# Optimization experiments

Measured on AMD Instinct MI355X. Metric: run time of the kernel, lower is better.

The kernel has to match this reference:

```python
import jax, jax.numpy as jnp
import numpy as np

N, M, P = 100000, 20000, 1600000          # nodes, hyperedges, incidence pairs
C_IN, HID, OUT = 768, 128, 16             # OUT = n_layers = n_classes
EPS = 1e-5


def setup_inputs() -> dict:
    key = jax.random.key(0)
    ks = jax.random.split(key, 8)
    X = jax.random.normal(ks[0], (N, C_IN), jnp.float32)
    v_idx = jax.random.randint(ks[1], (P,), 0, N)
    e_idx = jax.random.randint(ks[2], (P,), 0, M)
    # parameters
    W_enc = jax.random.normal(ks[3], (C_IN, HID), jnp.float32) / np.sqrt(C_IN).astype(np.float32)
    b_enc = jnp.zeros((HID,), jnp.float32)
    ln_g = jnp.ones((OUT, HID), jnp.float32)
    ln_b = jnp.zeros((OUT, HID), jnp.float32)
    Wt = jax.random.normal(ks[4], (OUT, HID, HID), jnp.float32) / np.sqrt(HID).astype(np.float32)
    bt = jnp.zeros((OUT, HID), jnp.float32)
    W_out = jax.random.normal(ks[5], (HID, OUT), jnp.float32) / np.sqrt(HID).astype(np.float32)
    b_out = jnp.zeros((OUT,), jnp.float32)
    return dict(X=X, v_idx=v_idx, e_idx=e_idx, W_enc=W_enc, b_enc=b_enc,
                ln_g=ln_g, ln_b=ln_b, Wt=Wt, bt=bt, W_out=W_out, b_out=b_out)


def reference(X, v_idx, e_idx, W_enc, b_enc, ln_g, ln_b, Wt, bt, W_out, b_out):
    seg = jax.ops.segment_sum
    ones = jnp.ones((P,), X.dtype)
    inv_ce = 1.0 / jnp.maximum(seg(ones, e_idx, num_segments=M), 1.0)  # 1/|e|
    inv_cv = 1.0 / jnp.maximum(seg(ones, v_idx, num_segments=N), 1.0)  # 1/deg(v)

    def layernorm(h, g, b):
        mu = jnp.mean(h, axis=-1, keepdims=True)
        var = jnp.var(h, axis=-1, keepdims=True)
        return (h - mu) * jax.lax.rsqrt(var + EPS) * g + b

    def v2v_mean(h):
        # vertex -> hyperedge mean, then hyperedge -> vertex mean (HGNN+)
        Xe = seg(h[v_idx], e_idx, num_segments=M) * inv_ce[:, None]   # [M, HID]
        return seg(Xe[e_idx], v_idx, num_segments=N) * inv_cv[:, None]  # [N, HID]

    x = X @ W_enc + b_enc  # node_encoder

    def step(x, params):
        g, b, W, bb = params
        h = jax.nn.relu(layernorm(x, g, b))  # res+ block: norm -> act -> dropout(eval noop)
        h = h @ W + bb                       # HGNNPConv theta
        h = v2v_mean(h)                      # hypergraph message passing
        h = jax.nn.relu(h)                   # conv act (conv dropout = eval noop)
        return x + h, None                   # residual

    x, _ = jax.lax.scan(step, x, (ln_g, ln_b, Wt, bt))
    return jax.nn.log_softmax(x @ W_out + b_out, axis=1)
```

## Files before the change

kernel.cpp:

```cpp
#include <hip/hip_runtime.h>
#include <cstdint>
#include <cstddef>

#define N_NODES 100000
#define M_EDGES 20000
#define P_PAIRS 1600000
#define CIN 768
#define HID 128
#define OUT_C 16
#define NLAYERS 16
#define LN_EPS 1e-5f

using half8  = __attribute__((ext_vector_type(8))) _Float16;
using half4v = __attribute__((ext_vector_type(4))) _Float16;
using half2v = __attribute__((ext_vector_type(2))) _Float16;
using f32x4  = __attribute__((ext_vector_type(4))) float;
using f32x2  = __attribute__((ext_vector_type(2))) float;

#if defined(__has_builtin)
#if __has_builtin(__builtin_amdgcn_cvt_pk_f32_fp8) && __has_builtin(__builtin_amdgcn_cvt_pk_fp8_f32)
#define HAVE_HW_FP8 1
#endif
#endif

#ifndef HAVE_HW_FP8
#include <hip/hip_fp8.h>
#endif


__device__ __forceinline__ void acc4w(float* acc, unsigned w) {
#ifdef HAVE_HW_FP8
    f32x2 lo = __builtin_amdgcn_cvt_pk_f32_fp8((int)w, false);
    f32x2 hi = __builtin_amdgcn_cvt_pk_f32_fp8((int)w, true);
    acc[0] += lo[0]; acc[1] += lo[1]; acc[2] += hi[0]; acc[3] += hi[1];
#else
#pragma unroll
    for (int i = 0; i < 4; i++) {
        __half_raw hr = __hip_cvt_fp8_to_halfraw((__hip_fp8_storage_t)((w >> (8 * i)) & 0xffu), __HIP_E4M3);
        acc[i] += __half2float(*(__half*)&hr);
    }
#endif
}

__device__ __forceinline__ void acc16v(float* acc, uint4 w) {
    acc4w(acc + 0,  w.x);
    acc4w(acc + 4,  w.y);
    acc4w(acc + 8,  w.z);
    acc4w(acc + 12, w.w);
}

__device__ __forceinline__ unsigned char f32_to_fp8(float v) {
#ifdef HAVE_HW_FP8
    return (unsigned char)(__builtin_amdgcn_cvt_pk_fp8_f32(v, v, 0, false) & 0xff);
#else
    return (unsigned char)__hip_cvt_float_to_fp8(v, __HIP_SATFINITE, __HIP_E4M3);
#endif
}

__device__ __forceinline__ unsigned short pack2_fp8(float a, float b) {
#ifdef HAVE_HW_FP8
    return (unsigned short)(__builtin_amdgcn_cvt_pk_fp8_f32(a, b, 0, false) & 0xffff);
#else
    return (unsigned short)((unsigned)f32_to_fp8(a) | ((unsigned)f32_to_fp8(b) << 8));
#endif
}

__device__ __forceinline__ unsigned pack4_fp8(float a, float b, float c, float d) {
#ifdef HAVE_HW_FP8
    int w = __builtin_amdgcn_cvt_pk_fp8_f32(a, b, 0, false);
    w = __builtin_amdgcn_cvt_pk_fp8_f32(c, d, w, true);
    return (unsigned)w;
#else
    return (unsigned)f32_to_fp8(a) | ((unsigned)f32_to_fp8(b) << 8) |
           ((unsigned)f32_to_fp8(c) << 16) | ((unsigned)f32_to_fp8(d) << 24);
#endif
}


__global__ void hist_kernel(const int* __restrict__ v_idx, const int* __restrict__ e_idx,
                            unsigned* __restrict__ cnt_v, unsigned* __restrict__ cnt_e) {
    int p = blockIdx.x * 256 + threadIdx.x;
    if (p < P_PAIRS) {
        atomicAdd(&cnt_v[v_idx[p]], 1u);
        atomicAdd(&cnt_e[e_idx[p]], 1u);
    }
}

#define SCAN_EPT 16
#define SCAN_CHUNK 4096

__global__ void scan_block_sums(const unsigned* __restrict__ cnt, int n,
                                unsigned* __restrict__ bsum) {
    __shared__ unsigned ws[4];
    int t = threadIdx.x;
    int base = blockIdx.x * SCAN_CHUNK + t * SCAN_EPT;
    unsigned s = 0;
#pragma unroll
    for (int i = 0; i < SCAN_EPT; i++) {
        int idx = base + i;
        if (idx < n) s += cnt[idx];
    }
#pragma unroll
    for (int off = 1; off < 64; off <<= 1) s += __shfl_xor(s, off);
    int lane = t & 63, w = t >> 6;
    if (lane == 0) ws[w] = s;
    __syncthreads();
    if (t == 0) bsum[blockIdx.x] = ws[0] + ws[1] + ws[2] + ws[3];
}

__global__ void scan_tops(const unsigned* __restrict__ bsum, int B,
                          unsigned* __restrict__ bbase, unsigned* __restrict__ total_out) {
    int t = threadIdx.x;
    unsigned v = (t < B) ? bsum[t] : 0u;
    unsigned s = v;
#pragma unroll
    for (int off = 1; off < 64; off <<= 1) {
        unsigned u = __shfl_up(s, off);
        if (t >= off) s += u;
    }
    if (t < B) bbase[t] = s - v;
    if (t == 63) *total_out = s;
}

__global__ void scan_final(const unsigned* __restrict__ cnt, int n,
                           const unsigned* __restrict__ bbase,
                           unsigned* __restrict__ offs, unsigned* __restrict__ cur,
                           float* __restrict__ inv) {
    __shared__ unsigned wtot[4];
    int t = threadIdx.x;
    int lane = t & 63, w = t >> 6;
    int base = blockIdx.x * SCAN_CHUNK + t * SCAN_EPT;
    unsigned vals[SCAN_EPT];
    unsigned tsum = 0;
#pragma unroll
    for (int i = 0; i < SCAN_EPT; i++) {
        int idx = base + i;
        unsigned v = (idx < n) ? cnt[idx] : 0u;
        vals[i] = v;
        tsum += v;
    }
    unsigned s = tsum;
#pragma unroll
    for (int off = 1; off < 64; off <<= 1) {
        unsigned u = __shfl_up(s, off);
        if (lane >= off) s += u;
    }
    unsigned texcl = s - tsum;
    if (lane == 63) wtot[w] = s;
    __syncthreads();
    unsigned wbase = 0;
    for (int i = 0; i < w; i++) wbase += wtot[i];
    unsigned run = bbase[blockIdx.x] + wbase + texcl;
#pragma unroll
    for (int i = 0; i < SCAN_EPT; i++) {
        int idx = base + i;
        if (idx < n) {
            offs[idx] = run;
            cur[idx] = run;
            unsigned c = vals[i];
            inv[idx] = 1.0f / (float)(c > 1u ? c : 1u);
            run += c;
        }
    }
}


__global__ void fill_v_kernel(const int* __restrict__ v_idx, const int* __restrict__ e_idx,
                              unsigned* __restrict__ cur_v, unsigned short* __restrict__ vert_nbr) {
    int p = blockIdx.x * 256 + threadIdx.x;
    if (p < P_PAIRS) {
        unsigned s = atomicAdd(&cur_v[v_idx[p]], 1u);
        vert_nbr[s] = (unsigned short)e_idx[p];
    }
}

__global__ void fill_e_kernel(const int* __restrict__ v_idx, const int* __restrict__ e_idx,
                              unsigned* __restrict__ cur_e, int* __restrict__ edge_nbr) {
    int p = blockIdx.x * 256 + threadIdx.x;
    if (p < P_PAIRS) {
        unsigned s = atomicAdd(&cur_e[e_idx[p]], 1u);
        edge_nbr[s] = v_idx[p];
    }
}


__global__ void convert_wT_kernel(const float* __restrict__ W, _Float16* __restrict__ WT,
                                  int K) {
    const float* src = W + (size_t)blockIdx.y * K * 128;
    _Float16* dst = WT + (size_t)blockIdx.y * K * 128;
    int idx = blockIdx.x * 256 + threadIdx.x;
    if (idx < K * 128) {
        int k = idx >> 7, n = idx & 127;
        dst[(size_t)n * K + k] = (_Float16)src[idx];
    }
}


#define BK  64
#define LDK 72

template<bool A_FP32, int OMODE>
__global__ __launch_bounds__(256) void mfma_gemm_kernel(
    const void* __restrict__ Ap, const _Float16* __restrict__ Bt,
    const float* __restrict__ bias, void* __restrict__ outp,
    int nrows, int K) {
    __shared__ _Float16 Asm[128 * LDK];
    __shared__ _Float16 Bsm[128 * LDK];
    int tid = threadIdx.x;
    int row0 = blockIdx.x * 128;
    int lane = tid & 63, wave = tid >> 6;
    int wy = wave >> 1, wx = wave & 1;
    int m16 = lane & 15, quad = lane >> 4;

    f32x4 acc[4][4];
#pragma unroll
    for (int r = 0; r < 4; r++)
#pragma unroll
        for (int c = 0; c < 4; c++) acc[r][c] = (f32x4)0.f;

    float bv[4];
#pragma unroll
    for (int c = 0; c < 4; c++) bv[c] = bias[wx * 64 + c * 16 + m16];

    for (int k0 = 0; k0 < K; k0 += BK) {
        __syncthreads();
        if (A_FP32) {
            const float* A = (const float*)Ap;
#pragma unroll
            for (int i = 0; i < 8; i++) {
                int idx = tid + i * 256;
                int r = idx >> 4, c = idx & 15;
                int rg = row0 + r; if (rg >= nrows) rg = nrows - 1;
                float4 v = *(const float4*)(A + (size_t)rg * K + k0 + c * 4);
                half4v h = { (_Float16)v.x, (_Float16)v.y, (_Float16)v.z, (_Float16)v.w };
                *(half4v*)&Asm[r * LDK + c * 4] = h;
            }
        } else {
            const _Float16* A = (const _Float16*)Ap;
#pragma unroll
            for (int i = 0; i < 4; i++) {
                int idx = tid + i * 256;
                int r = idx >> 3, c = idx & 7;
                int rg = row0 + r; if (rg >= nrows) rg = nrows - 1;
                half8 v = *(const half8*)(A + (size_t)rg * K + k0 + c * 8);
                *(half8*)&Asm[r * LDK + c * 8] = v;
            }
        }
#pragma unroll
        for (int i = 0; i < 4; i++) {
            int idx = tid + i * 256;
            int r = idx >> 3, c = idx & 7;
            half8 v = *(const half8*)(Bt + (size_t)r * K + k0 + c * 8);
            *(half8*)&Bsm[r * LDK + c * 8] = v;
        }
        __syncthreads();
#pragma unroll
        for (int ks = 0; ks < 2; ks++) {
            half8 af[4], bf[4];
#pragma unroll
            for (int r = 0; r < 4; r++)
                af[r] = *(half8*)&Asm[(wy * 64 + r * 16 + m16) * LDK + ks * 32 + quad * 8];
#pragma unroll
            for (int c = 0; c < 4; c++)
                bf[c] = *(half8*)&Bsm[(wx * 64 + c * 16 + m16) * LDK + ks * 32 + quad * 8];
#pragma unroll
            for (int r = 0; r < 4; r++)
#pragma unroll
                for (int c = 0; c < 4; c++)
                    acc[r][c] = __builtin_amdgcn_mfma_f32_16x16x32_f16(af[r], bf[c], acc[r][c], 0, 0, 0);
        }
    }
#pragma unroll
    for (int r = 0; r < 4; r++) {
#pragma unroll
        for (int v = 0; v < 4; v++) {
            int m = wy * 64 + r * 16 + quad * 4 + v;
            int row = row0 + m;
            if (row < nrows) {
#pragma unroll
                for (int c = 0; c < 4; c++) {
                    int n = wx * 64 + c * 16 + m16;
                    float val = acc[r][c][v] + bv[c];
                    if (OMODE == 0) {
                        ((float*)outp)[(size_t)row * HID + n] = val;
                    } else {
                        ((unsigned char*)outp)[(size_t)row * HID + n] = f32_to_fp8(val);
                    }
                }
            }
        }
    }
}


__global__ __launch_bounds__(256) void ln_relu_kernel(const float* __restrict__ x,
                                                      const float* __restrict__ g,
                                                      const float* __restrict__ b,
                                                      unsigned char* __restrict__ a8) {
    int row = (blockIdx.x * 256 + threadIdx.x) >> 6;
    int lane = threadIdx.x & 63;
    if (row >= N_NODES) return;
    float2 v = *(const float2*)(x + (size_t)row * HID + 2 * lane);
    float s = v.x + v.y;
#pragma unroll
    for (int off = 1; off < 64; off <<= 1) s += __shfl_xor(s, off);
    float mu = s * (1.0f / 128.0f);
    float d0 = v.x - mu, d1 = v.y - mu;
    float q = d0 * d0 + d1 * d1;
#pragma unroll
    for (int off = 1; off < 64; off <<= 1) q += __shfl_xor(q, off);
    float rstd = rsqrtf(q * (1.0f / 128.0f) + LN_EPS);
    float2 gg = *(const float2*)(g + 2 * lane);
    float2 bb = *(const float2*)(b + 2 * lane);
    float h0 = fmaxf(d0 * rstd * gg.x + bb.x, 0.f);
    float h1 = fmaxf(d1 * rstd * gg.y + bb.y, 0.f);
    *(unsigned short*)(a8 + (size_t)row * HID + 2 * lane) = pack2_fp8(h0, h1);
}


__global__ __launch_bounds__(256) void edge_agg_kernel(const unsigned char* __restrict__ a8,
                                                       const int* __restrict__ edge_nbr,
                                                       const unsigned* __restrict__ offs,
                                                       const float* __restrict__ inv_ce,
                                                       _Float16* __restrict__ Ae) {
    int m = blockIdx.x * 4 + (threadIdx.x >> 6);
    int lane = threadIdx.x & 63;
    int g = lane >> 3, t = lane & 7;
    unsigned beg = offs[m], end = offs[m + 1];
    float acc[16];
#pragma unroll
    for (int i = 0; i < 16; i++) acc[i] = 0.f;
    const unsigned char* base = a8 + t * 16;
    unsigned j = beg;
    for (; j + 16 <= end; j += 16) {
        int v0 = edge_nbr[j + g];
        int v1 = edge_nbr[j + 8 + g];
        uint4 w0 = *(const uint4*)(base + (size_t)v0 * HID);
        uint4 w1 = *(const uint4*)(base + (size_t)v1 * HID);
        acc16v(acc, w0);
        acc16v(acc, w1);
    }
    if (j + 8 <= end) {
        int v0 = edge_nbr[j + g];
        uint4 w0 = *(const uint4*)(base + (size_t)v0 * HID);
        acc16v(acc, w0);
        j += 8;
    }
    if (j < end) {
        unsigned idx = j + g;
        bool val = idx < end;
        int v0 = edge_nbr[val ? idx : beg];
        uint4 w = *(const uint4*)(base + (size_t)v0 * HID);
        if (!val) { w.x = 0; w.y = 0; w.z = 0; w.w = 0; }
        acc16v(acc, w);
    }
#pragma unroll
    for (int i = 0; i < 16; i++) {
        acc[i] += __shfl_xor(acc[i], 8);
        acc[i] += __shfl_xor(acc[i], 16);
        acc[i] += __shfl_xor(acc[i], 32);
    }
    if (lane < 8) {
        float ic = inv_ce[m];
        half8 o0, o1;
#pragma unroll
        for (int i = 0; i < 8; i++) o0[i] = (_Float16)(acc[i] * ic);
#pragma unroll
        for (int i = 0; i < 8; i++) o1[i] = (_Float16)(acc[8 + i] * ic);
        *(half8*)(Ae + (size_t)m * HID + t * 16) = o0;
        *(half8*)(Ae + (size_t)m * HID + t * 16 + 8) = o1;
    }
}


__global__ __launch_bounds__(256) void vert_fused_kernel(
    const unsigned char* __restrict__ Xe8, const unsigned short* __restrict__ vert_nbr,
    const unsigned* __restrict__ offs, const float* __restrict__ inv_cv,
    float* __restrict__ x, const float* __restrict__ gw, const float* __restrict__ bw,
    unsigned char* __restrict__ a8, int do_ln) {
    int v = blockIdx.x * 4 + (threadIdx.x >> 6);
    int lane = threadIdx.x & 63;
    int g = lane >> 3, t = lane & 7;
    unsigned beg = offs[v], end = offs[v + 1];
    float acc[16];
#pragma unroll
    for (int i = 0; i < 16; i++) acc[i] = 0.f;
    const unsigned char* base = Xe8 + t * 16;
    unsigned j = beg;
    for (; j + 16 <= end; j += 16) {
        int e0 = vert_nbr[j + g];
        int e1 = vert_nbr[j + 8 + g];
        uint4 w0 = *(const uint4*)(base + (size_t)e0 * HID);
        uint4 w1 = *(const uint4*)(base + (size_t)e1 * HID);
        acc16v(acc, w0);
        acc16v(acc, w1);
    }
    if (j + 8 <= end) {
        int e0 = vert_nbr[j + g];
        uint4 w0 = *(const uint4*)(base + (size_t)e0 * HID);
        acc16v(acc, w0);
        j += 8;
    }
    if (j < end) {
        unsigned idx = j + g;
        bool val = idx < end;
        int e0 = vert_nbr[val ? idx : beg];
        uint4 w = *(const uint4*)(base + (size_t)e0 * HID);
        if (!val) { w.x = 0; w.y = 0; w.z = 0; w.w = 0; }
        acc16v(acc, w);
    }
#pragma unroll
    for (int i = 0; i < 16; i++) {
        acc[i] += __shfl_xor(acc[i], 8);
        acc[i] += __shfl_xor(acc[i], 16);
        acc[i] += __shfl_xor(acc[i], 32);
    }
    if (lane < 8) {
        float ic = inv_cv[v];
        float xv[16];
        f32x4* xp = (f32x4*)(x + (size_t)v * HID + t * 16);
        f32x4 xa = xp[0], xb = xp[1], xc = xp[2], xd = xp[3];
#pragma unroll
        for (int i = 0; i < 4; i++) { xv[i] = xa[i]; xv[4 + i] = xb[i]; xv[8 + i] = xc[i]; xv[12 + i] = xd[i]; }
#pragma unroll
        for (int i = 0; i < 16; i++) xv[i] += fmaxf(acc[i] * ic, 0.f);
#pragma unroll
        for (int i = 0; i < 4; i++) { xa[i] = xv[i]; xb[i] = xv[4 + i]; xc[i] = xv[8 + i]; xd[i] = xv[12 + i]; }
        xp[0] = xa; xp[1] = xb; xp[2] = xc; xp[3] = xd;
        if (do_ln) {
            float s = 0.f;
#pragma unroll
            for (int i = 0; i < 16; i++) s += xv[i];
#pragma unroll
            for (int off = 1; off < 8; off <<= 1) s += __shfl_xor(s, off);
            float mu = s * (1.0f / 128.0f);
            float d[16];
            float q = 0.f;
#pragma unroll
            for (int i = 0; i < 16; i++) { d[i] = xv[i] - mu; q += d[i] * d[i]; }
#pragma unroll
            for (int off = 1; off < 8; off <<= 1) q += __shfl_xor(q, off);
            float rstd = rsqrtf(q * (1.0f / 128.0f) + LN_EPS);
            const f32x4* gp = (const f32x4*)(gw + t * 16);
            const f32x4* bp = (const f32x4*)(bw + t * 16);
            float o[16];
#pragma unroll
            for (int k = 0; k < 4; k++) {
                f32x4 gg = gp[k], bb = bp[k];
#pragma unroll
                for (int i = 0; i < 4; i++)
                    o[k * 4 + i] = fmaxf(d[k * 4 + i] * rstd * gg[i] + bb[i], 0.f);
            }
            uint4 pk;
            pk.x = pack4_fp8(o[0],  o[1],  o[2],  o[3]);
            pk.y = pack4_fp8(o[4],  o[5],  o[6],  o[7]);
            pk.z = pack4_fp8(o[8],  o[9],  o[10], o[11]);
            pk.w = pack4_fp8(o[12], o[13], o[14], o[15]);
            *(uint4*)(a8 + (size_t)v * HID + t * 16) = pk;
        }
    }
}


__global__ __launch_bounds__(256) void out_kernel(const float* __restrict__ x,
                                                  const float* __restrict__ Wo,
                                                  const float* __restrict__ bo,
                                                  float* __restrict__ out) {
    __shared__ float Ws[128][16];
    __shared__ float rowbuf[16][132];
    __shared__ float bsm[16];
    int tid = threadIdx.x;
#pragma unroll
    for (int i = 0; i < 8; i++) {
        int idx = tid + i * 256;
        ((float*)Ws)[idx] = Wo[idx];
    }
    if (tid < 16) bsm[tid] = bo[tid];
    int row0 = blockIdx.x * 16;
    int w = tid >> 6, lane = tid & 63;
#pragma unroll
    for (int i = 0; i < 8; i++) {
        int idx = lane + i * 64;
        int r = idx >> 7, k = idx & 127;
        int row = row0 + w * 4 + r;
        rowbuf[w * 4 + r][k] = (row < N_NODES) ? x[(size_t)row * HID + k] : 0.f;
    }
    __syncthreads();
    int r = lane >> 4, c = lane & 15;
    int row = row0 + w * 4 + r;
    float acc = bsm[c];
#pragma unroll
    for (int k = 0; k < 128; k++) acc += rowbuf[w * 4 + r][k] * Ws[k][c];
    float mx = acc;
#pragma unroll
    for (int off = 1; off < 16; off <<= 1) mx = fmaxf(mx, __shfl_xor(mx, off));
    float e = expf(acc - mx);
    float s = e;
#pragma unroll
    for (int off = 1; off < 16; off <<= 1) s += __shfl_xor(s, off);
    float val = acc - mx - logf(s);
    if (row < N_NODES) out[(size_t)row * OUT_C + c] = val;
}


extern "C" void kernel_launch(void* const* d_in, const int* in_sizes, int n_in,
                              void* d_out, int out_size, void* d_ws, size_t ws_size,
                              hipStream_t stream) {
    const float* X     = (const float*)d_in[0];
    const int*   v_idx = (const int*)d_in[1];
    const int*   e_idx = (const int*)d_in[2];
    const float* W_enc = (const float*)d_in[3];
    const float* b_enc = (const float*)d_in[4];
    const float* ln_g  = (const float*)d_in[5];
    const float* ln_b  = (const float*)d_in[6];
    const float* Wt    = (const float*)d_in[7];
    const float* bt    = (const float*)d_in[8];
    const float* W_out = (const float*)d_in[9];
    const float* b_out = (const float*)d_in[10];
    float* out = (float*)d_out;

    char* ws = (char*)d_ws;
    auto alloc = [&](size_t bytes) -> void* {
        void* p = (void*)ws;
        ws += (bytes + 255) & ~(size_t)255;
        return p;
    };
    float*    x       = (float*)alloc((size_t)N_NODES * HID * 4);
    unsigned char* a8 = (unsigned char*)alloc((size_t)N_NODES * HID);
    _Float16* Ae_h    = (_Float16*)alloc((size_t)M_EDGES * HID * 2);
    unsigned char* Xe8 = (unsigned char*)alloc((size_t)M_EDGES * HID);
    _Float16* WencT_h = (_Float16*)alloc((size_t)CIN * HID * 2);
    _Float16* WtT_h   = (_Float16*)alloc((size_t)NLAYERS * HID * HID * 2);
    int* edge_nbr = (int*)alloc((size_t)P_PAIRS * 4);
    unsigned short* vert_nbr = (unsigned short*)alloc((size_t)P_PAIRS * 2);
    unsigned* cnt_e = (unsigned*)alloc((size_t)(M_EDGES + N_NODES) * 4);
    unsigned* cnt_v = cnt_e + M_EDGES;
    unsigned* offs_e = (unsigned*)alloc((size_t)(M_EDGES + 1) * 4);
    unsigned* offs_v = (unsigned*)alloc((size_t)(N_NODES + 1) * 4);
    unsigned* cur_e  = (unsigned*)alloc((size_t)M_EDGES * 4);
    unsigned* cur_v  = (unsigned*)alloc((size_t)N_NODES * 4);
    float* inv_ce = (float*)alloc((size_t)M_EDGES * 4);
    float* inv_cv = (float*)alloc((size_t)N_NODES * 4);
    unsigned* bsum_e = (unsigned*)alloc(64 * 4);
    unsigned* bbase_e = (unsigned*)alloc(64 * 4);
    unsigned* bsum_v = (unsigned*)alloc(64 * 4);
    unsigned* bbase_v = (unsigned*)alloc(64 * 4);

    const int BE = (M_EDGES + SCAN_CHUNK - 1) / SCAN_CHUNK;
    const int BV = (N_NODES + SCAN_CHUNK - 1) / SCAN_CHUNK;

    hipMemsetAsync(cnt_e, 0, (size_t)(M_EDGES + N_NODES) * 4, stream);
    hist_kernel<<<(P_PAIRS + 255) / 256, 256, 0, stream>>>(v_idx, e_idx, cnt_v, cnt_e);
    scan_block_sums<<<BE, 256, 0, stream>>>(cnt_e, M_EDGES, bsum_e);
    scan_tops<<<1, 64, 0, stream>>>(bsum_e, BE, bbase_e, offs_e + M_EDGES);
    scan_final<<<BE, 256, 0, stream>>>(cnt_e, M_EDGES, bbase_e, offs_e, cur_e, inv_ce);
    scan_block_sums<<<BV, 256, 0, stream>>>(cnt_v, N_NODES, bsum_v);
    scan_tops<<<1, 64, 0, stream>>>(bsum_v, BV, bbase_v, offs_v + N_NODES);
    scan_final<<<BV, 256, 0, stream>>>(cnt_v, N_NODES, bbase_v, offs_v, cur_v, inv_cv);
    fill_v_kernel<<<(P_PAIRS + 255) / 256, 256, 0, stream>>>(v_idx, e_idx, cur_v, vert_nbr);
    fill_e_kernel<<<(P_PAIRS + 255) / 256, 256, 0, stream>>>(v_idx, e_idx, cur_e, edge_nbr);

    {
        dim3 g1((CIN * HID + 255) / 256, 1);
        convert_wT_kernel<<<g1, 256, 0, stream>>>(W_enc, WencT_h, CIN);
        dim3 g2((HID * HID + 255) / 256, NLAYERS);
        convert_wT_kernel<<<g2, 256, 0, stream>>>(Wt, WtT_h, HID);
    }

    mfma_gemm_kernel<true, 0><<<(N_NODES + 127) / 128, 256, 0, stream>>>(
        (const void*)X, WencT_h, b_enc, (void*)x, N_NODES, CIN);

    ln_relu_kernel<<<(N_NODES * 64 + 255) / 256, 256, 0, stream>>>(
        x, ln_g, ln_b, a8);

    for (int l = 0; l < NLAYERS; l++) {
        edge_agg_kernel<<<M_EDGES / 4, 256, 0, stream>>>(a8, edge_nbr, offs_e, inv_ce, Ae_h);
        mfma_gemm_kernel<false, 1><<<(M_EDGES + 127) / 128, 256, 0, stream>>>(
            (const void*)Ae_h, WtT_h + (size_t)l * HID * HID, bt + l * HID,
            (void*)Xe8, M_EDGES, HID);
        int lnext = (l + 1 < NLAYERS) ? (l + 1) : (NLAYERS - 1);
        vert_fused_kernel<<<N_NODES / 4, 256, 0, stream>>>(
            Xe8, vert_nbr, offs_v, inv_cv, x,
            ln_g + (size_t)lnext * HID, ln_b + (size_t)lnext * HID, a8,
            (l + 1 < NLAYERS) ? 1 : 0);
    }

    out_kernel<<<(N_NODES + 15) / 16, 256, 0, stream>>>(x, W_out, b_out, out);
}
```

Baseline: 2.576 ms.

## Split fp8 node activations into 32-column chunks for cache-friendly edge gather

Stores the fp8 normalized node activations as four column-chunk planes of 32 bytes per node instead of one 128-byte row. The edge aggregation kernel gains a grid dimension over chunks, so each pass gathers from a 3.2 MB plane that fits in L2/MALL rather than the full 12.8 MB array. Index, residual and output accesses are also switched to nontemporal loads and stores. In exchange the edge neighbor list is read four times and each gathered access is only 32 bytes wide.

```diff
diff --git a/kernel.cpp b/kernel.cpp
--- a/kernel.cpp
+++ b/kernel.cpp
@@ -10,12 +10,15 @@
 #define OUT_C 16
 #define NLAYERS 16
 #define LN_EPS 1e-5f
+#define NCHUNK 4
+#define CW 32
 
 using half8  = __attribute__((ext_vector_type(8))) _Float16;
 using half4v = __attribute__((ext_vector_type(4))) _Float16;
 using half2v = __attribute__((ext_vector_type(2))) _Float16;
 using f32x4  = __attribute__((ext_vector_type(4))) float;
 using f32x2  = __attribute__((ext_vector_type(2))) float;
+using u32x4  = __attribute__((ext_vector_type(4))) unsigned int;
 
 #if defined(__has_builtin)
 #if __has_builtin(__builtin_amdgcn_cvt_pk_f32_fp8) && __has_builtin(__builtin_amdgcn_cvt_pk_fp8_f32)
@@ -42,11 +45,11 @@
 #endif
 }
 
-__device__ __forceinline__ void acc16v(float* acc, uint4 w) {
-    acc4w(acc + 0,  w.x);
-    acc4w(acc + 4,  w.y);
-    acc4w(acc + 8,  w.z);
-    acc4w(acc + 12, w.w);
+__device__ __forceinline__ void acc16v(float* acc, u32x4 w) {
+    acc4w(acc + 0,  w[0]);
+    acc4w(acc + 4,  w[1]);
+    acc4w(acc + 8,  w[2]);
+    acc4w(acc + 12, w[3]);
 }
 
 __device__ __forceinline__ unsigned char f32_to_fp8(float v) {
@@ -314,61 +317,67 @@
     float2 bb = *(const float2*)(b + 2 * lane);
     float h0 = fmaxf(d0 * rstd * gg.x + bb.x, 0.f);
     float h1 = fmaxf(d1 * rstd * gg.y + bb.y, 0.f);
-    *(unsigned short*)(a8 + (size_t)row * HID + 2 * lane) = pack2_fp8(h0, h1);
-}
-
-
-__global__ __launch_bounds__(256) void edge_agg_kernel(const unsigned char* __restrict__ a8,
-                                                       const int* __restrict__ edge_nbr,
-                                                       const unsigned* __restrict__ offs,
-                                                       const float* __restrict__ inv_ce,
-                                                       _Float16* __restrict__ Ae) {
+    int c = lane >> 4;
+    int off2 = (2 * lane) & 31;
+    *(unsigned short*)(a8 + (size_t)c * ((size_t)N_NODES * CW) + (size_t)row * CW + off2) =
+        pack2_fp8(h0, h1);
+}
+
+
+__global__ __launch_bounds__(256) void edge_agg_chunk_kernel(
+    const unsigned char* __restrict__ a8, const int* __restrict__ edge_nbr,
+    const unsigned* __restrict__ offs, const float* __restrict__ inv_ce,
+    _Float16* __restrict__ Ae) {
     int m = blockIdx.x * 4 + (threadIdx.x >> 6);
+    int c = blockIdx.y;
     int lane = threadIdx.x & 63;
-    int g = lane >> 3, t = lane & 7;
+    int r32 = lane >> 1, t2 = lane & 1;
     unsigned beg = offs[m], end = offs[m + 1];
     float acc[16];
 #pragma unroll
     for (int i = 0; i < 16; i++) acc[i] = 0.f;
-    const unsigned char* base = a8 + t * 16;
+    const unsigned char* base = a8 + (size_t)c * ((size_t)N_NODES * CW) + t2 * 16;
     unsigned j = beg;
-    for (; j + 16 <= end; j += 16) {
-        int v0 = edge_nbr[j + g];
-        int v1 = edge_nbr[j + 8 + g];
-        uint4 w0 = *(const uint4*)(base + (size_t)v0 * HID);
-        uint4 w1 = *(const uint4*)(base + (size_t)v1 * HID);
+    for (; j + 64 <= end; j += 64) {
+        int v0 = __builtin_nontemporal_load(&edge_nbr[j + r32]);
+        int v1 = __builtin_nontemporal_load(&edge_nbr[j + 32 + r32]);
+        u32x4 w0 = *(const u32x4*)(base + (size_t)v0 * CW);
+        u32x4 w1 = *(const u32x4*)(base + (size_t)v1 * CW);
         acc16v(acc, w0);
         acc16v(acc, w1);
     }
-    if (j + 8 <= end) {
-        int v0 = edge_nbr[j + g];
-        uint4 w0 = *(const uint4*)(base + (size_t)v0 * HID);
+    if (j + 32 <= end) {
+        int v0 = __builtin_nontemporal_load(&edge_nbr[j + r32]);
+        u32x4 w0 = *(const u32x4*)(base + (size_t)v0 * CW);
         acc16v(acc, w0);
-        j += 8;
+        j += 32;
     }
     if (j < end) {
-        unsigned idx = j + g;
+        unsigned idx = j + r32;
         bool val = idx < end;
-        int v0 = edge_nbr[val ? idx : beg];
-        uint4 w = *(const uint4*)(base + (size_t)v0 * HID);
-        if (!val) { w.x = 0; w.y = 0; w.z = 0; w.w = 0; }
+        int v0 = __builtin_nontemporal_load(&edge_nbr[val ? idx : beg]);
+        u32x4 w = *(const u32x4*)(base + (size_t)v0 * CW);
+        if (!val) w = (u32x4)0u;
         acc16v(acc, w);
     }
 #pragma unroll
     for (int i = 0; i < 16; i++) {
+        acc[i] += __shfl_xor(acc[i], 2);
+        acc[i] += __shfl_xor(acc[i], 4);
         acc[i] += __shfl_xor(acc[i], 8);
         acc[i] += __shfl_xor(acc[i], 16);
         acc[i] += __shfl_xor(acc[i], 32);
     }
-    if (lane < 8) {
+    if (r32 == 0) {
         float ic = inv_ce[m];
         half8 o0, o1;
 #pragma unroll
         for (int i = 0; i < 8; i++) o0[i] = (_Float16)(acc[i] * ic);
 #pragma unroll
         for (int i = 0; i < 8; i++) o1[i] = (_Float16)(acc[8 + i] * ic);
-        *(half8*)(Ae + (size_t)m * HID + t * 16) = o0;
-        *(half8*)(Ae + (size_t)m * HID + t * 16 + 8) = o1;
+        _Float16* dst = Ae + (size_t)m * HID + c * CW + t2 * 16;
+        __builtin_nontemporal_store(o0, (half8*)dst);
+        __builtin_nontemporal_store(o1, (half8*)(dst + 8));
     }
 }
 
@@ -388,25 +397,25 @@
     const unsigned char* base = Xe8 + t * 16;
     unsigned j = beg;
     for (; j + 16 <= end; j += 16) {
-        int e0 = vert_nbr[j + g];
-        int e1 = vert_nbr[j + 8 + g];
-        uint4 w0 = *(const uint4*)(base + (size_t)e0 * HID);
-        uint4 w1 = *(const uint4*)(base + (size_t)e1 * HID);
+        int e0 = __builtin_nontemporal_load(&vert_nbr[j + g]);
+        int e1 = __builtin_nontemporal_load(&vert_nbr[j + 8 + g]);
+        u32x4 w0 = *(const u32x4*)(base + (size_t)e0 * HID);
+        u32x4 w1 = *(const u32x4*)(base + (size_t)e1 * HID);
         acc16v(acc, w0);
         acc16v(acc, w1);
     }
     if (j + 8 <= end) {
-        int e0 = vert_nbr[j + g];
-        uint4 w0 = *(const uint4*)(base + (size_t)e0 * HID);
+        int e0 = __builtin_nontemporal_load(&vert_nbr[j + g]);
+        u32x4 w0 = *(const u32x4*)(base + (size_t)e0 * HID);
         acc16v(acc, w0);
         j += 8;
     }
     if (j < end) {
         unsigned idx = j + g;
         bool val = idx < end;
-        int e0 = vert_nbr[val ? idx : beg];
-        uint4 w = *(const uint4*)(base + (size_t)e0 * HID);
-        if (!val) { w.x = 0; w.y = 0; w.z = 0; w.w = 0; }
+        int e0 = __builtin_nontemporal_load(&vert_nbr[val ? idx : beg]);
+        u32x4 w = *(const u32x4*)(base + (size_t)e0 * HID);
+        if (!val) w = (u32x4)0u;
         acc16v(acc, w);
     }
 #pragma unroll
@@ -419,14 +428,20 @@
         float ic = inv_cv[v];
         float xv[16];
         f32x4* xp = (f32x4*)(x + (size_t)v * HID + t * 16);
-        f32x4 xa = xp[0], xb = xp[1], xc = xp[2], xd = xp[3];
+        f32x4 xa = __builtin_nontemporal_load(xp);
+        f32x4 xb = __builtin_nontemporal_load(xp + 1);
+        f32x4 xc = __builtin_nontemporal_load(xp + 2);
+        f32x4 xd = __builtin_nontemporal_load(xp + 3);
 #pragma unroll
         for (int i = 0; i < 4; i++) { xv[i] = xa[i]; xv[4 + i] = xb[i]; xv[8 + i] = xc[i]; xv[12 + i] = xd[i]; }
 #pragma unroll
         for (int i = 0; i < 16; i++) xv[i] += fmaxf(acc[i] * ic, 0.f);
 #pragma unroll
         for (int i = 0; i < 4; i++) { xa[i] = xv[i]; xb[i] = xv[4 + i]; xc[i] = xv[8 + i]; xd[i] = xv[12 + i]; }
-        xp[0] = xa; xp[1] = xb; xp[2] = xc; xp[3] = xd;
+        __builtin_nontemporal_store(xa, xp);
+        __builtin_nontemporal_store(xb, xp + 1);
+        __builtin_nontemporal_store(xc, xp + 2);
+        __builtin_nontemporal_store(xd, xp + 3);
         if (do_ln) {
             float s = 0.f;
 #pragma unroll
@@ -451,12 +466,14 @@
                 for (int i = 0; i < 4; i++)
                     o[k * 4 + i] = fmaxf(d[k * 4 + i] * rstd * gg[i] + bb[i], 0.f);
             }
-            uint4 pk;
-            pk.x = pack4_fp8(o[0],  o[1],  o[2],  o[3]);
-            pk.y = pack4_fp8(o[4],  o[5],  o[6],  o[7]);
-            pk.z = pack4_fp8(o[8],  o[9],  o[10], o[11]);
-            pk.w = pack4_fp8(o[12], o[13], o[14], o[15]);
-            *(uint4*)(a8 + (size_t)v * HID + t * 16) = pk;
+            u32x4 pk;
+            pk[0] = pack4_fp8(o[0],  o[1],  o[2],  o[3]);
+            pk[1] = pack4_fp8(o[4],  o[5],  o[6],  o[7]);
+            pk[2] = pack4_fp8(o[8],  o[9],  o[10], o[11]);
+            pk[3] = pack4_fp8(o[12], o[13], o[14], o[15]);
+            u32x4* dst = (u32x4*)(a8 + (size_t)(t >> 1) * ((size_t)N_NODES * CW) +
+                                  (size_t)v * CW + (t & 1) * 16);
+            __builtin_nontemporal_store(pk, dst);
         }
     }
 }
@@ -574,7 +591,8 @@
         x, ln_g, ln_b, a8);
 
     for (int l = 0; l < NLAYERS; l++) {
-        edge_agg_kernel<<<M_EDGES / 4, 256, 0, stream>>>(a8, edge_nbr, offs_e, inv_ce, Ae_h);
+        dim3 ge(M_EDGES / 4, NCHUNK);
+        edge_agg_chunk_kernel<<<ge, 256, 0, stream>>>(a8, edge_nbr, offs_e, inv_ce, Ae_h);
         mfma_gemm_kernel<false, 1><<<(M_EDGES + 127) / 128, 256, 0, stream>>>(
             (const void*)Ae_h, WtT_h + (size_t)l * HID * HID, bt + l * HID,
             (void*)Xe8, M_EDGES, HID);
```

New measurement: 3.490 ms. +35.5%, slower.

## Remap vertex gather to 16 lanes per vertex with persistent grid-stride loop

Applied to the files above, without the earlier changes.

The vertex aggregation kernel now assigns 16 lanes per vertex (4 vertices per wave), each lane owning 8 feature bytes, instead of one vertex per wave split into 8 neighbour groups. This removes the cross-lane reduction of 16 accumulators and keeps all lanes busy in the residual and layernorm epilogue. The launch becomes a fixed 2048-block persistent grid with the LN parameters hoisted out of the loop. The trade-off is longer serial neighbour loops per lane with smaller 8-byte loads, and the index reads are repeated by every lane in a group.

```diff
diff --git a/kernel.cpp b/kernel.cpp
--- a/kernel.cpp
+++ b/kernel.cpp
@@ -10,12 +10,15 @@
 #define OUT_C 16
 #define NLAYERS 16
 #define LN_EPS 1e-5f
+#define VBLOCKS 2048
 
 using half8  = __attribute__((ext_vector_type(8))) _Float16;
 using half4v = __attribute__((ext_vector_type(4))) _Float16;
 using half2v = __attribute__((ext_vector_type(2))) _Float16;
 using f32x4  = __attribute__((ext_vector_type(4))) float;
 using f32x2  = __attribute__((ext_vector_type(2))) float;
+using u32x2  = __attribute__((ext_vector_type(2))) unsigned int;
+using u32x4  = __attribute__((ext_vector_type(4))) unsigned int;
 
 #if defined(__has_builtin)
 #if __has_builtin(__builtin_amdgcn_cvt_pk_f32_fp8) && __has_builtin(__builtin_amdgcn_cvt_pk_fp8_f32)
@@ -42,11 +45,11 @@
 #endif
 }
 
-__device__ __forceinline__ void acc16v(float* acc, uint4 w) {
-    acc4w(acc + 0,  w.x);
-    acc4w(acc + 4,  w.y);
-    acc4w(acc + 8,  w.z);
-    acc4w(acc + 12, w.w);
+__device__ __forceinline__ void acc16v(float* acc, u32x4 w) {
+    acc4w(acc + 0,  w[0]);
+    acc4w(acc + 4,  w[1]);
+    acc4w(acc + 8,  w[2]);
+    acc4w(acc + 12, w[3]);
 }
 
 __device__ __forceinline__ unsigned char f32_to_fp8(float v) {
@@ -335,14 +338,14 @@
     for (; j + 16 <= end; j += 16) {
         int v0 = edge_nbr[j + g];
         int v1 = edge_nbr[j + 8 + g];
-        uint4 w0 = *(const uint4*)(base + (size_t)v0 * HID);
-        uint4 w1 = *(const uint4*)(base + (size_t)v1 * HID);
+        u32x4 w0 = *(const u32x4*)(base + (size_t)v0 * HID);
+        u32x4 w1 = *(const u32x4*)(base + (size_t)v1 * HID);
         acc16v(acc, w0);
         acc16v(acc, w1);
     }
     if (j + 8 <= end) {
         int v0 = edge_nbr[j + g];
-        uint4 w0 = *(const uint4*)(base + (size_t)v0 * HID);
+        u32x4 w0 = *(const u32x4*)(base + (size_t)v0 * HID);
         acc16v(acc, w0);
         j += 8;
     }
@@ -350,8 +353,8 @@
         unsigned idx = j + g;
         bool val = idx < end;
         int v0 = edge_nbr[val ? idx : beg];
-        uint4 w = *(const uint4*)(base + (size_t)v0 * HID);
-        if (!val) { w.x = 0; w.y = 0; w.z = 0; w.w = 0; }
+        u32x4 w = *(const u32x4*)(base + (size_t)v0 * HID);
+        if (!val) w = (u32x4)0u;
         acc16v(acc, w);
     }
 #pragma unroll
@@ -378,85 +381,78 @@
     const unsigned* __restrict__ offs, const float* __restrict__ inv_cv,
     float* __restrict__ x, const float* __restrict__ gw, const float* __restrict__ bw,
     unsigned char* __restrict__ a8, int do_ln) {
-    int v = blockIdx.x * 4 + (threadIdx.x >> 6);
+    int wave_id = blockIdx.x * 4 + (threadIdx.x >> 6);
     int lane = threadIdx.x & 63;
-    int g = lane >> 3, t = lane & 7;
-    unsigned beg = offs[v], end = offs[v + 1];
-    float acc[16];
-#pragma unroll
-    for (int i = 0; i < 16; i++) acc[i] = 0.f;
-    const unsigned char* base = Xe8 + t * 16;
-    unsigned j = beg;
-    for (; j + 16 <= end; j += 16) {
-        int e0 = vert_nbr[j + g];
-        int e1 = vert_nbr[j + 8 + g];
-        uint4 w0 = *(const uint4*)(base + (size_t)e0 * HID);
-        uint4 w1 = *(const uint4*)(base + (size_t)e1 * HID);
-        acc16v(acc, w0);
-        acc16v(acc, w1);
-    }
-    if (j + 8 <= end) {
-        int e0 = vert_nbr[j + g];
-        uint4 w0 = *(const uint4*)(base + (size_t)e0 * HID);
-        acc16v(acc, w0);
-        j += 8;
-    }
-    if (j < end) {
-        unsigned idx = j + g;
-        bool val = idx < end;
-        int e0 = vert_nbr[val ? idx : beg];
-        uint4 w = *(const uint4*)(base + (size_t)e0 * HID);
-        if (!val) { w.x = 0; w.y = 0; w.z = 0; w.w = 0; }
-        acc16v(acc, w);
-    }
-#pragma unroll
-    for (int i = 0; i < 16; i++) {
-        acc[i] += __shfl_xor(acc[i], 8);
-        acc[i] += __shfl_xor(acc[i], 16);
-        acc[i] += __shfl_xor(acc[i], 32);
-    }
-    if (lane < 8) {
+    int t = lane & 15;
+    const unsigned char* base = Xe8 + t * 8;
+
+    f32x2 g01 = {0.f, 0.f};
+    f32x4 gg0, gg1, bb0, bb1;
+    if (do_ln) {
+        gg0 = *(const f32x4*)(gw + t * 8);
+        gg1 = *(const f32x4*)(gw + t * 8 + 4);
+        bb0 = *(const f32x4*)(bw + t * 8);
+        bb1 = *(const f32x4*)(bw + t * 8 + 4);
+    }
+    (void)g01;
+
+    for (int v = wave_id * 4 + (lane >> 4); v < N_NODES; v += VBLOCKS * 16) {
+        unsigned beg = offs[v], end = offs[v + 1];
+        float acc[8] = {0.f, 0.f, 0.f, 0.f, 0.f, 0.f, 0.f, 0.f};
+        unsigned j = beg;
+        for (; j + 4 <= end; j += 4) {
+            int e0 = vert_nbr[j];
+            int e1 = vert_nbr[j + 1];
+            int e2 = vert_nbr[j + 2];
+            int e3 = vert_nbr[j + 3];
+            u32x2 w0 = *(const u32x2*)(base + (size_t)e0 * HID);
+            u32x2 w1 = *(const u32x2*)(base + (size_t)e1 * HID);
+            u32x2 w2 = *(const u32x2*)(base + (size_t)e2 * HID);
+            u32x2 w3 = *(const u32x2*)(base + (size_t)e3 * HID);
+            acc4w(acc, w0[0]); acc4w(acc + 4, w0[1]);
+            acc4w(acc, w1[0]); acc4w(acc + 4, w1[1]);
+            acc4w(acc, w2[0]); acc4w(acc + 4, w2[1]);
+            acc4w(acc, w3[0]); acc4w(acc + 4, w3[1]);
+        }
+        for (; j < end; j++) {
+            int e0 = vert_nbr[j];
+            u32x2 w0 = *(const u32x2*)(base + (size_t)e0 * HID);
+            acc4w(acc, w0[0]); acc4w(acc + 4, w0[1]);
+        }
         float ic = inv_cv[v];
-        float xv[16];
-        f32x4* xp = (f32x4*)(x + (size_t)v * HID + t * 16);
-        f32x4 xa = xp[0], xb = xp[1], xc = xp[2], xd = xp[3];
-#pragma unroll
-        for (int i = 0; i < 4; i++) { xv[i] = xa[i]; xv[4 + i] = xb[i]; xv[8 + i] = xc[i]; xv[12 + i] = xd[i]; }
-#pragma unroll
-        for (int i = 0; i < 16; i++) xv[i] += fmaxf(acc[i] * ic, 0.f);
-#pragma unroll
-        for (int i = 0; i < 4; i++) { xa[i] = xv[i]; xb[i] = xv[4 + i]; xc[i] = xv[8 + i]; xd[i] = xv[12 + i]; }
-        xp[0] = xa; xp[1] = xb; xp[2] = xc; xp[3] = xd;
+        float xv[8];
+        f32x4* xp = (f32x4*)(x + (size_t)v * HID + t * 8);
+        f32x4 xa = xp[0], xb = xp[1];
+#pragma unroll
+        for (int i = 0; i < 4; i++) { xv[i] = xa[i]; xv[4 + i] = xb[i]; }
+#pragma unroll
+        for (int i = 0; i < 8; i++) xv[i] += fmaxf(acc[i] * ic, 0.f);
+#pragma unroll
+        for (int i = 0; i < 4; i++) { xa[i] = xv[i]; xb[i] = xv[4 + i]; }
+        xp[0] = xa; xp[1] = xb;
         if (do_ln) {
             float s = 0.f;
 #pragma unroll
-            for (int i = 0; i < 16; i++) s += xv[i];
-#pragma unroll
-            for (int off = 1; off < 8; off <<= 1) s += __shfl_xor(s, off);
+            for (int i = 0; i < 8; i++) s += xv[i];
+#pragma unroll
+            for (int off = 1; off < 16; off <<= 1) s += __shfl_xor(s, off);
             float mu = s * (1.0f / 128.0f);
-            float d[16];
+            float d[8];
             float q = 0.f;
 #pragma unroll
-            for (int i = 0; i < 16; i++) { d[i] = xv[i] - mu; q += d[i] * d[i]; }
-#pragma unroll
-            for (int off = 1; off < 8; off <<= 1) q += __shfl_xor(q, off);
+            for (int i = 0; i < 8; i++) { d[i] = xv[i] - mu; q += d[i] * d[i]; }
+#pragma unroll
+            for (int off = 1; off < 16; off <<= 1) q += __shfl_xor(q, off);
             float rstd = rsqrtf(q * (1.0f / 128.0f) + LN_EPS);
-            const f32x4* gp = (const f32x4*)(gw + t * 16);
-            const f32x4* bp = (const f32x4*)(bw + t * 16);
-            float o[16];
-#pragma unroll
-            for (int k = 0; k < 4; k++) {
-                f32x4 gg = gp[k], bb = bp[k];
-#pragma unroll
-                for (int i = 0; i < 4; i++)
-                    o[k * 4 + i] = fmaxf(d[k * 4 + i] * rstd * gg[i] + bb[i], 0.f);
-            }
-            uint4 pk;
-            pk.x = pack4_fp8(o[0],  o[1],  o[2],  o[3]);
-            pk.y = pack4_fp8(o[4],  o[5],  o[6],  o[7]);
-            pk.z = pack4_fp8(o[8],  o[9],  o[10], o[11]);
-            pk.w = pack4_fp8(o[12], o[13], o[14], o[15]);
-            *(uint4*)(a8 + (size_t)v * HID + t * 16) = pk;
+            float o[8];
+#pragma unroll
+            for (int i = 0; i < 4; i++) o[i]     = fmaxf(d[i]     * rstd * gg0[i] + bb0[i], 0.f);
+#pragma unroll
+            for (int i = 0; i < 4; i++) o[4 + i] = fmaxf(d[4 + i] * rstd * gg1[i] + bb1[i], 0.f);
+            u32x2 pk;
+            pk[0] = pack4_fp8(o[0], o[1], o[2], o[3]);
+            pk[1] = pack4_fp8(o[4], o[5], o[6], o[7]);
+            *(u32x2*)(a8 + (size_t)v * HID + t * 8) = pk;
         }
     }
 }
@@ -579,7 +575,7 @@
             (const void*)Ae_h, WtT_h + (size_t)l * HID * HID, bt + l * HID,
             (void*)Xe8, M_EDGES, HID);
         int lnext = (l + 1 < NLAYERS) ? (l + 1) : (NLAYERS - 1);
-        vert_fused_kernel<<<N_NODES / 4, 256, 0, stream>>>(
+        vert_fused_kernel<<<VBLOCKS, 256, 0, stream>>>(
             Xe8, vert_nbr, offs_v, inv_cv, x,
             ln_g + (size_t)lnext * HID, ln_b + (size_t)lnext * HID, a8,
             (l + 1 < NLAYERS) ? 1 : 0);
```

New measurement: 2.212 ms. -14.1%, faster.
